# Performance work log

Hardware: AMD Instinct MI355X
Metric: run time of the kernel (lower is better)

The kernel has to match this reference:

```python
import jax, jax.numpy as jnp
import numpy as np

E = 7       # number of experts (len(expert_details))
K = 2       # top-k routing
CAP = 3072  # per-expert capacity ~ ceil(T*K/E * 1.25)
D = 1024    # d_model
H = 4096    # d_ff = 4*d_model
T = 8192    # tokens (B=2, S=4096)


def setup_inputs() -> dict:
    key = jax.random.key(0)
    k1, k2, k3, k4 = jax.random.split(key, 4)
    x = jax.random.normal(k1, (T, D), jnp.float32)
    Wg = jax.random.normal(k2, (D, E), jnp.float32) * 0.02
    W1 = jax.random.normal(k3, (E, D, H), jnp.float32) * 0.02
    W2 = jax.random.normal(k4, (E, H, D), jnp.float32) * 0.02
    return {"x": x, "Wg": Wg, "W1": W1, "W2": W2}


def reference(x, Wg, W1, W2):
    Tn, Dn = x.shape
    # --- router ---
    gates = jax.nn.softmax(x @ Wg, axis=-1)          # [T, E]
    topw, topi = jax.lax.top_k(gates, K)             # [T, K]
    topw = topw / jnp.sum(topw, axis=-1, keepdims=True)
    flat_e = topi.reshape(-1)                        # [T*K] expert ids (int)
    flat_w = topw.reshape(-1)                        # [T*K] combine weights
    # --- position within each expert (priority = token order) ---
    onehot = jax.nn.one_hot(flat_e, E, dtype=jnp.int32)           # [T*K, E]
    pos = jnp.sum(jnp.cumsum(onehot, axis=0) * onehot, axis=-1) - 1  # [T*K]
    keep = pos < CAP
    slot = jnp.where(keep, pos, CAP)  # overflow tokens go to pad slot CAP
    # --- dispatch: scatter tokens into [E, CAP, D] buffer ---
    x_rep = jnp.repeat(x, K, axis=0)                               # [T*K, D]
    buf = jnp.zeros((E, CAP + 1, Dn), x.dtype).at[flat_e, slot].set(x_rep)[:, :CAP]
    # --- grouped expert FFN (grouped GEMMs) ---
    h = jax.nn.gelu(jnp.einsum('ecd,edh->ech', buf, W1))
    y = jnp.einsum('ech,ehd->ecd', h, W2)                          # [E, CAP, D]
    # --- combine: gather back and weight ---
    y_pad = jnp.concatenate([y, jnp.zeros((E, 1, Dn), y.dtype)], axis=1)
    out_slots = y_pad[flat_e, slot] * (flat_w * keep.astype(flat_w.dtype))[:, None]
    return out_slots.reshape(Tn, K, Dn).sum(axis=1)                # [T, D]
```

## Files before the change

### kernel.cpp

```cpp
#include <hip/hip_runtime.h>
#include <stdint.h>


#define NEXP 7
#define KTOP 2
#define CAP 3072
#define DM 1024
#define HF 4096
#define TT 8192
#define RBLK 32

typedef __bf16 bf16x8 __attribute__((ext_vector_type(8)));
typedef float f32x4 __attribute__((ext_vector_type(4)));

__device__ __forceinline__ unsigned short f2bf(float v) {
  union { float f; unsigned u; } a; a.f = v;
  unsigned r = a.u + 0x7FFFu + ((a.u >> 16) & 1u);
  return (unsigned short)(r >> 16);
}
__device__ __forceinline__ float bf2f(unsigned short h) {
  union { unsigned u; float f; } a; a.u = ((unsigned)h) << 16; return a.f;
}
__device__ __forceinline__ float gelu_t(float v) {
  float u = 0.7978845608028654f * (v + 0.044715f * v * v * v);
  float ex = __expf(2.0f * u);
  float th = 1.0f - 2.0f / (ex + 1.0f);
  return 0.5f * v * (1.0f + th);
}
__device__ __forceinline__ void gl2lds16(const void* g, void* l) {
  __builtin_amdgcn_global_load_lds(
      (const __attribute__((address_space(1))) unsigned int*)g,
      (__attribute__((address_space(3))) unsigned int*)l, 16, 0, 0);
}

__global__ void init_counts(int* counts) {
  if (threadIdx.x < NEXP) counts[threadIdx.x] = 0;
}

__global__ __launch_bounds__(256) void router_fused(
    const float* __restrict__ x, const float* __restrict__ Wg,
    int* __restrict__ counts, int* __restrict__ flatSlot,
    int* __restrict__ tokOfSlot, float* __restrict__ wOfSlot,
    unsigned short* __restrict__ xb) {
  __shared__ float sWgT[NEXP][DM];
  __shared__ int hist[NEXP], base[NEXP];
  __shared__ int pickE[RBLK * 2];
  __shared__ int pickR[RBLK * 2];
  __shared__ float pickW[RBLK * 2];
  int tid = threadIdx.x, lane = tid & 63, wave = tid >> 6;

  for (int i = tid; i < NEXP * DM; i += 256) {
    int e = i / DM, d = i - e * DM;
    sWgT[e][d] = Wg[d * NEXP + e];
  }
  if (tid < NEXP) hist[tid] = 0;
  __syncthreads();

  for (int tt = wave; tt < RBLK; tt += 4) {
    int t = blockIdx.x * RBLK + tt;
    const float4* xr = (const float4*)(x + (long)t * DM);
    double acc[NEXP];
#pragma unroll
    for (int e = 0; e < NEXP; ++e) acc[e] = 0.0;
#pragma unroll
    for (int j = 0; j < 4; ++j) {
      float4 xv = xr[j * 64 + lane];
      int d4 = (j * 64 + lane) * 4;
#pragma unroll
      for (int e = 0; e < NEXP; ++e) {
        float4 wv = *(const float4*)&sWgT[e][d4];
        acc[e] += (double)xv.x * (double)wv.x + (double)xv.y * (double)wv.y
                + (double)xv.z * (double)wv.z + (double)xv.w * (double)wv.w;
      }
    }
#pragma unroll
    for (int e = 0; e < NEXP; ++e) {
#pragma unroll
      for (int off = 32; off > 0; off >>= 1) acc[e] += __shfl_down(acc[e], off);
    }
    if (lane == 0) {
      int i1 = 0; double l1 = acc[0];
      for (int e2 = 1; e2 < NEXP; ++e2) if (acc[e2] > l1) { l1 = acc[e2]; i1 = e2; }
      int i2 = -1; double l2 = -1e300;
      for (int e2 = 0; e2 < NEXP; ++e2) if (e2 != i1 && acc[e2] > l2) { l2 = acc[e2]; i2 = e2; }
      float w1 = (float)(1.0 / (1.0 + exp(l2 - l1)));
      int r0 = atomicAdd(&hist[i1], 1);
      int r1 = atomicAdd(&hist[i2], 1);
      pickE[2 * tt] = i1;     pickR[2 * tt] = r0;     pickW[2 * tt] = w1;
      pickE[2 * tt + 1] = i2; pickR[2 * tt + 1] = r1; pickW[2 * tt + 1] = 1.0f - w1;
    }
  }
  __syncthreads();
  if (tid < NEXP) base[tid] = atomicAdd(&counts[tid], hist[tid]);
  __syncthreads();

  for (int tt = wave; tt < RBLK; tt += 4) {
    int t = blockIdx.x * RBLK + tt;
    const float4* xr = (const float4*)(x + (long)t * DM);
    float4 v0 = xr[0 * 64 + lane], v1 = xr[1 * 64 + lane];
    float4 v2 = xr[2 * 64 + lane], v3 = xr[3 * 64 + lane];
    ushort4 o0, o1, o2, o3;
    o0.x = f2bf(v0.x); o0.y = f2bf(v0.y); o0.z = f2bf(v0.z); o0.w = f2bf(v0.w);
    o1.x = f2bf(v1.x); o1.y = f2bf(v1.y); o1.z = f2bf(v1.z); o1.w = f2bf(v1.w);
    o2.x = f2bf(v2.x); o2.y = f2bf(v2.y); o2.z = f2bf(v2.z); o2.w = f2bf(v2.w);
    o3.x = f2bf(v3.x); o3.y = f2bf(v3.y); o3.z = f2bf(v3.z); o3.w = f2bf(v3.w);
#pragma unroll
    for (int p = 0; p < 2; ++p) {
      int e = pickE[2 * tt + p];
      int s = base[e] + pickR[2 * tt + p];
      int fi = t * 2 + p;
      if (lane == 0) {
        flatSlot[fi] = (s < CAP) ? s : CAP;
        if (s < CAP) { tokOfSlot[e * CAP + s] = fi; wOfSlot[e * CAP + s] = pickW[2 * tt + p]; }
      }
      if (s < CAP) {
        ushort4* dst = (ushort4*)(xb + ((long)e * CAP + s) * DM);
        dst[0 * 64 + lane] = o0; dst[1 * 64 + lane] = o1;
        dst[2 * 64 + lane] = o2; dst[3 * 64 + lane] = o3;
      }
    }
  }
}

__global__ void transcvt(const float* __restrict__ in, unsigned short* __restrict__ out,
                         int R, int C) {
  __shared__ float tile[64][65];
  long base = (long)blockIdx.z * (long)R * (long)C;
  const float* inp = in + base;
  unsigned short* outp = out + base;
  int c0 = blockIdx.x * 64, r0 = blockIdx.y * 64;
  int lx = threadIdx.x & 63, ly = threadIdx.x >> 6;
#pragma unroll
  for (int i = 0; i < 16; ++i) {
    int r = ly + i * 4;
    tile[r][lx] = inp[(long)(r0 + r) * C + c0 + lx];
  }
  __syncthreads();
#pragma unroll
  for (int i = 0; i < 16; ++i) {
    int c = ly + i * 4;
    outp[(long)(c0 + c) * R + r0 + lx] = f2bf(tile[lx][c]);
  }
}

template <int EPI>
__global__ __launch_bounds__(512, 2) void gemm256(
    const unsigned short* __restrict__ A, const unsigned short* __restrict__ Bt,
    void* __restrict__ Cout, const int* __restrict__ counts,
    const int* __restrict__ tokOfSlot, const float* __restrict__ wOfSlot,
    int LD, int klen, int N, int kspl, long aexps, long cexps) {
  __shared__ __align__(16) unsigned short sAb[2][16384];
  __shared__ __align__(16) unsigned short sBb[2][16384];
  int e = blockIdx.z / kspl, ks = blockIdx.z % kspl;
  int mcnt = counts[e]; mcnt = mcnt < CAP ? mcnt : CAP;
  int m0 = blockIdx.y * 256;
  if (m0 >= mcnt) return;
  int n0 = blockIdx.x * 256;
  long kstart = (long)ks * klen;

  const unsigned short* Ae = A + (long)e * aexps;
  const unsigned short* Be = Bt + (long)e * (long)N * LD;

  int tid = threadIdx.x;
  int lane = tid & 63, wave = tid >> 6;
  int wr = wave >> 2, wc = wave & 3;
  int lm = lane & 15, quad = lane >> 4;

  int srow = tid >> 3;
  int scol = ((lane & 7) ^ (lane >> 3)) << 3;
  const unsigned short* As = Ae + (long)(m0 + srow) * LD + kstart + scol;
  const unsigned short* Bs = Be + (long)(n0 + srow) * LD + kstart + scol;

  int abase = (wr * 128 + lm) * 64;
  int bbase = (wc * 64 + lm) * 64;
  int cx0 = (quad ^ (lm & 7)) << 3;
  int cx1 = ((quad + 4) ^ (lm & 7)) << 3;

  f32x4 acc[8][4];
#pragma unroll
  for (int i = 0; i < 8; ++i)
#pragma unroll
    for (int j = 0; j < 4; ++j) acc[i][j] = f32x4{0.f, 0.f, 0.f, 0.f};

  int NT = klen >> 6, NI = NT >> 1;

#define STA(buf, kt, half) do { \
    int _kt = (kt) < NT ? (kt) : (NT - 1); \
    gl2lds16(As + (long)_kt * 64 + (long)((half) * 2) * 64 * LD, \
             &sAb[buf][(half) * 8192 + tid * 8]); \
    gl2lds16(As + (long)_kt * 64 + (long)((half) * 2 + 1) * 64 * LD, \
             &sAb[buf][(half) * 8192 + 4096 + tid * 8]); \
  } while (0)
#define STB(buf, kt, half) do { \
    int _kt = (kt) < NT ? (kt) : (NT - 1); \
    gl2lds16(Bs + (long)_kt * 64 + (long)((half) * 2) * 64 * LD, \
             &sBb[buf][(half) * 8192 + tid * 8]); \
    gl2lds16(Bs + (long)_kt * 64 + (long)((half) * 2 + 1) * 64 * LD, \
             &sBb[buf][(half) * 8192 + 4096 + tid * 8]); \
  } while (0)

  bf16x8 bF[4][2];

#define PHASE(buf, mi0, RB, STAGE, VM) do { \
    bf16x8 a00 = *(const bf16x8*)&sAb[buf][abase + (mi0) * 1024 + cx0]; \
    bf16x8 a01 = *(const bf16x8*)&sAb[buf][abase + (mi0) * 1024 + cx1]; \
    bf16x8 a10 = *(const bf16x8*)&sAb[buf][abase + (mi0) * 1024 + 1024 + cx0]; \
    bf16x8 a11 = *(const bf16x8*)&sAb[buf][abase + (mi0) * 1024 + 1024 + cx1]; \
    if (RB) { \
      _Pragma("unroll") \
      for (int ni = 0; ni < 4; ++ni) { \
        bF[ni][0] = *(const bf16x8*)&sBb[buf][bbase + ni * 1024 + cx0]; \
        bF[ni][1] = *(const bf16x8*)&sBb[buf][bbase + ni * 1024 + cx1]; \
      } \
    } \
    STAGE; \
    __builtin_amdgcn_s_barrier(); \
    asm volatile("s_waitcnt lgkmcnt(0)" ::: "memory"); \
    __builtin_amdgcn_sched_barrier(0); \
    __builtin_amdgcn_s_setprio(1); \
    _Pragma("unroll") \
    for (int ni = 0; ni < 4; ++ni) { \
      acc[mi0][ni]     = __builtin_amdgcn_mfma_f32_16x16x32_bf16(a00, bF[ni][0], acc[mi0][ni], 0, 0, 0); \
      acc[mi0][ni]     = __builtin_amdgcn_mfma_f32_16x16x32_bf16(a01, bF[ni][1], acc[mi0][ni], 0, 0, 0); \
      acc[mi0 + 1][ni] = __builtin_amdgcn_mfma_f32_16x16x32_bf16(a10, bF[ni][0], acc[mi0 + 1][ni], 0, 0, 0); \
      acc[mi0 + 1][ni] = __builtin_amdgcn_mfma_f32_16x16x32_bf16(a11, bF[ni][1], acc[mi0 + 1][ni], 0, 0, 0); \
    } \
    __builtin_amdgcn_s_setprio(0); \
    VM; \
    __builtin_amdgcn_s_barrier(); \
  } while (0)

  STA(0, 0, 0); STA(0, 0, 1); STB(0, 0, 0); STB(0, 0, 1);
  STB(1, 1, 0); STB(1, 1, 1);
  asm volatile("s_waitcnt vmcnt(4)" ::: "memory");
  __builtin_amdgcn_s_barrier();

  for (int t = 0; t < NI; ++t) {
    int k0 = 2 * t, k1 = 2 * t + 1;
    PHASE(0, 0, 1, STA(1, k1, 0), (void)0);
    PHASE(0, 2, 0, STA(1, k1, 1), (void)0);
    PHASE(0, 4, 0, STB(0, k0 + 2, 0), (void)0);
    PHASE(0, 6, 0, STB(0, k0 + 2, 1),
          asm volatile("s_waitcnt vmcnt(4)" ::: "memory"));
    PHASE(1, 0, 1, STA(0, k0 + 2, 0), (void)0);
    PHASE(1, 2, 0, STA(0, k0 + 2, 1), (void)0);
    PHASE(1, 4, 0, STB(1, k1 + 2, 0), (void)0);
    PHASE(1, 6, 0, STB(1, k1 + 2, 1),
          asm volatile("s_waitcnt vmcnt(4)" ::: "memory"));
  }
  asm volatile("s_waitcnt vmcnt(0)" ::: "memory");
#undef PHASE
#undef STA
#undef STB

  if (EPI == 0) {
    unsigned short* Ce = (unsigned short*)Cout + (long)e * cexps;
#pragma unroll
    for (int mi = 0; mi < 8; ++mi) {
      int mb = m0 + wr * 128 + mi * 16 + quad * 4;
#pragma unroll
      for (int r = 0; r < 4; ++r) {
        int m = mb + r;
        if (m < mcnt) {
#pragma unroll
          for (int ni = 0; ni < 4; ++ni) {
            int n = n0 + wc * 64 + ni * 16 + lm;
            Ce[(long)m * N + n] = f2bf(gelu_t(acc[mi][ni][r]));
          }
        }
      }
    }
  } else {
    unsigned short* Y = (unsigned short*)Cout + (long)ks * ((long)TT * KTOP * DM);
#pragma unroll
    for (int mi = 0; mi < 8; ++mi) {
      int mb = m0 + wr * 128 + mi * 16 + quad * 4;
#pragma unroll
      for (int r = 0; r < 4; ++r) {
        int m = mb + r;
        if (m < mcnt) {
          int fi = tokOfSlot[e * CAP + m];
          float w = wOfSlot[e * CAP + m];
#pragma unroll
          for (int ni = 0; ni < 4; ++ni) {
            int n = n0 + wc * 64 + ni * 16 + lm;
            Y[(long)fi * N + n] = f2bf(w * acc[mi][ni][r]);
          }
        }
      }
    }
  }
}

template <int EPI>
__global__ __launch_bounds__(256, 2) void gemm_bt(
    const unsigned short* __restrict__ A, const unsigned short* __restrict__ Bt,
    void* __restrict__ Cout, const int* __restrict__ counts,
    const int* __restrict__ tokOfSlot, const float* __restrict__ wOfSlot,
    int K, int N, int eoff, long aexps, long cexps) {
  __shared__ unsigned short sA[128 * 32];
  __shared__ unsigned short sB[128 * 32];
  int e = eoff + blockIdx.z;
  int mcnt = counts[e]; mcnt = mcnt < CAP ? mcnt : CAP;
  int m0 = blockIdx.y * 128;
  if (m0 >= mcnt) return;
  int n0 = blockIdx.x * 128;
  const unsigned short* Ae = A + (long)blockIdx.z * aexps;
  const unsigned short* Be = Bt + (long)e * (long)N * (long)K;

  int tid = threadIdx.x;
  int lane = tid & 63, wave = tid >> 6;
  int lm = lane & 15, quad = lane >> 4;
  int wm = (wave & 1) * 64, wn = (wave >> 1) * 64;

  int ra = tid >> 2;
  int ca = (tid & 3) * 8;
  const unsigned short* Ab0 = Ae + (long)(m0 + ra) * K + ca;
  const unsigned short* Ab1 = Ae + (long)(m0 + 64 + ra) * K + ca;
  const unsigned short* Bb0 = Be + (long)(n0 + ra) * K + ca;
  const unsigned short* Bb1 = Be + (long)(n0 + 64 + ra) * K + ca;
  unsigned short* sAp0 = &sA[tid * 8];
  unsigned short* sAp1 = &sA[(tid + 256) * 8];
  unsigned short* sBp0 = &sB[tid * 8];
  unsigned short* sBp1 = &sB[(tid + 256) * 8];

  f32x4 acc[4][4];
#pragma unroll
  for (int i = 0; i < 4; ++i)
#pragma unroll
    for (int j = 0; j < 4; ++j) acc[i][j] = f32x4{0.f, 0.f, 0.f, 0.f};

  for (int k0 = 0; k0 < K; k0 += 32) {
    gl2lds16(Ab0 + k0, sAp0);
    gl2lds16(Ab1 + k0, sAp1);
    gl2lds16(Bb0 + k0, sBp0);
    gl2lds16(Bb1 + k0, sBp1);
    __syncthreads();
    bf16x8 aF[4], bFf[4];
#pragma unroll
    for (int mi = 0; mi < 4; ++mi)
      aF[mi] = *(const bf16x8*)&sA[(wm + mi * 16 + lm) * 32 + quad * 8];
#pragma unroll
    for (int ni = 0; ni < 4; ++ni)
      bFf[ni] = *(const bf16x8*)&sB[(wn + ni * 16 + lm) * 32 + quad * 8];
#pragma unroll
    for (int mi = 0; mi < 4; ++mi)
#pragma unroll
      for (int ni = 0; ni < 4; ++ni)
        acc[mi][ni] = __builtin_amdgcn_mfma_f32_16x16x32_bf16(aF[mi], bFf[ni], acc[mi][ni], 0, 0, 0);
    __syncthreads();
  }

  if (EPI == 0) {
    unsigned short* Ce = (unsigned short*)Cout + (long)blockIdx.z * cexps;
#pragma unroll
    for (int mi = 0; mi < 4; ++mi) {
      int mb = m0 + wm + mi * 16 + quad * 4;
#pragma unroll
      for (int r = 0; r < 4; ++r) {
        int m = mb + r;
        if (m < mcnt) {
#pragma unroll
          for (int ni = 0; ni < 4; ++ni) {
            int n = n0 + wn + ni * 16 + lm;
            Ce[(long)m * N + n] = f2bf(gelu_t(acc[mi][ni][r]));
          }
        }
      }
    }
  } else {
    unsigned short* Y = (unsigned short*)Cout;
#pragma unroll
    for (int mi = 0; mi < 4; ++mi) {
      int mb = m0 + wm + mi * 16 + quad * 4;
#pragma unroll
      for (int r = 0; r < 4; ++r) {
        int m = mb + r;
        if (m < mcnt) {
          int fi = tokOfSlot[e * CAP + m];
          float w = wOfSlot[e * CAP + m];
#pragma unroll
          for (int ni = 0; ni < 4; ++ni) {
            int n = n0 + wn + ni * 16 + lm;
            Y[(long)fi * N + n] = f2bf(w * acc[mi][ni][r]);
          }
        }
      }
    }
  }
}

__global__ void combine_k2(const unsigned short* __restrict__ yflat,
                           const int* __restrict__ flatSlot, float* __restrict__ out) {
  int t = blockIdx.x;
  bool k0 = flatSlot[2 * t] < CAP, k1 = flatSlot[2 * t + 1] < CAP;
  const long S = (long)TT * KTOP * DM;
  const ushort4* y00 = (const ushort4*)(yflat + (long)(2 * t) * DM);
  const ushort4* y01 = (const ushort4*)(yflat + S + (long)(2 * t) * DM);
  const ushort4* y10 = (const ushort4*)(yflat + (long)(2 * t + 1) * DM);
  const ushort4* y11 = (const ushort4*)(yflat + S + (long)(2 * t + 1) * DM);
  ushort4 a = y00[threadIdx.x], a2 = y01[threadIdx.x];
  ushort4 b = y10[threadIdx.x], b2 = y11[threadIdx.x];
  float4 r;
  r.x = (k0 ? bf2f(a.x) + bf2f(a2.x) : 0.f) + (k1 ? bf2f(b.x) + bf2f(b2.x) : 0.f);
  r.y = (k0 ? bf2f(a.y) + bf2f(a2.y) : 0.f) + (k1 ? bf2f(b.y) + bf2f(b2.y) : 0.f);
  r.z = (k0 ? bf2f(a.z) + bf2f(a2.z) : 0.f) + (k1 ? bf2f(b.z) + bf2f(b2.z) : 0.f);
  r.w = (k0 ? bf2f(a.w) + bf2f(a2.w) : 0.f) + (k1 ? bf2f(b.w) + bf2f(b2.w) : 0.f);
  ((float4*)(out + (long)t * DM))[threadIdx.x] = r;
}

__global__ void combine_k(const unsigned short* __restrict__ yflat,
                          const int* __restrict__ flatSlot, float* __restrict__ out) {
  int t = blockIdx.x;
  bool k0 = flatSlot[2 * t] < CAP, k1 = flatSlot[2 * t + 1] < CAP;
  const ushort4* y0 = (const ushort4*)(yflat + (long)(2 * t) * DM);
  const ushort4* y1 = (const ushort4*)(yflat + (long)(2 * t + 1) * DM);
  ushort4 a = y0[threadIdx.x], b = y1[threadIdx.x];
  float4 r;
  r.x = (k0 ? bf2f(a.x) : 0.f) + (k1 ? bf2f(b.x) : 0.f);
  r.y = (k0 ? bf2f(a.y) : 0.f) + (k1 ? bf2f(b.y) : 0.f);
  r.z = (k0 ? bf2f(a.z) : 0.f) + (k1 ? bf2f(b.z) : 0.f);
  r.w = (k0 ? bf2f(a.w) : 0.f) + (k1 ? bf2f(b.w) : 0.f);
  ((float4*)(out + (long)t * DM))[threadIdx.x] = r;
}

extern "C" void kernel_launch(void* const* d_in, const int* in_sizes, int n_in,
                              void* d_out, int out_size, void* d_ws, size_t ws_size,
                              hipStream_t stream) {
  const float* x  = (const float*)d_in[0];
  const float* Wg = (const float*)d_in[1];
  const float* W1 = (const float*)d_in[2];
  const float* W2 = (const float*)d_in[3];
  float* out = (float*)d_out;

  char* ws = (char*)d_ws;
  size_t off = 0;
  auto alloc = [&](size_t b) { void* p = ws + off; off = (off + b + 255) & ~(size_t)255; return p; };
  int* counts            = (int*)alloc(NEXP * 4);
  int* flatSlot          = (int*)alloc((size_t)TT * KTOP * 4);
  int* tokOfSlot         = (int*)alloc((size_t)NEXP * CAP * 4);
  float* wOfSlot         = (float*)alloc((size_t)NEXP * CAP * 4);
  unsigned short* Wb1    = (unsigned short*)alloc((size_t)NEXP * DM * HF * 2);
  unsigned short* Wb2    = (unsigned short*)alloc((size_t)NEXP * DM * HF * 2);
  unsigned short* xb     = (unsigned short*)alloc((size_t)NEXP * CAP * DM * 2);
  unsigned short* yflat  = (unsigned short*)alloc((size_t)2 * TT * KTOP * DM * 2);
  size_t hbA = (size_t)NEXP * CAP * HF * 2;
  size_t hbB = (size_t)CAP * HF * 2;
  int planA = (off + hbA) <= ws_size;
  unsigned short* hb = (unsigned short*)alloc(planA ? hbA : hbB);

  init_counts<<<1, 64, 0, stream>>>(counts);
  router_fused<<<TT / RBLK, 256, 0, stream>>>(x, Wg, counts, flatSlot, tokOfSlot, wOfSlot, xb);
  transcvt<<<dim3(HF / 64, DM / 64, NEXP), 256, 0, stream>>>(W1, Wb1, DM, HF);
  transcvt<<<dim3(DM / 64, HF / 64, NEXP), 256, 0, stream>>>(W2, Wb2, HF, DM);

  if (planA) {
    gemm256<0><<<dim3(HF / 256, CAP / 256, NEXP), 512, 0, stream>>>(
        xb, Wb1, hb, counts, tokOfSlot, wOfSlot, DM, DM, HF, 1,
        (long)CAP * DM, (long)CAP * HF);
    gemm256<1><<<dim3(DM / 256, CAP / 256, NEXP * 2), 512, 0, stream>>>(
        hb, Wb2, yflat, counts, tokOfSlot, wOfSlot, HF, HF / 2, DM, 2,
        (long)CAP * HF, 0);
    combine_k2<<<TT, 256, 0, stream>>>(yflat, flatSlot, out);
  } else {
    for (int e = 0; e < NEXP; ++e) {
      gemm_bt<0><<<dim3(HF / 128, CAP / 128, 1), 256, 0, stream>>>(
          xb + (size_t)e * CAP * DM, Wb1, hb, counts, tokOfSlot, wOfSlot, DM, HF, e, 0, 0);
      gemm_bt<1><<<dim3(DM / 128, CAP / 128, 1), 256, 0, stream>>>(
          hb, Wb2, yflat, counts, tokOfSlot, wOfSlot, HF, DM, e, 0, 0);
    }
    combine_k<<<TT, 256, 0, stream>>>(yflat, flatSlot, out);
  }
}
```

Before: 782.6 us.

## Fuse combine into second expert GEMM via fp32 atomic adds to output

The second grouped GEMM's epilogue now atomically adds the weighted fp32 results straight into a pre-zeroed output row for each token, so the bf16 split-K staging buffer and the separate combine kernel are no longer needed. The weight transpose-convert kernel now writes four bf16 values per store instead of one, and a scheduling barrier is removed from the MFMA phase macro. The aim is to cut intermediate memory traffic and a kernel launch. In exchange it adds contended atomics, order-dependent summation, and a zeroing pass.

```diff
diff --git a/kernel.cpp b/kernel.cpp
--- a/kernel.cpp
+++ b/kernel.cpp
@@ -35,6 +35,10 @@
 
 __global__ void init_counts(int* counts) {
   if (threadIdx.x < NEXP) counts[threadIdx.x] = 0;
+}
+
+__global__ void zero_out(float* __restrict__ out) {
+  ((float4*)(out + (long)blockIdx.x * DM))[threadIdx.x] = float4{0.f, 0.f, 0.f, 0.f};
 }
 
 __global__ __launch_bounds__(256) void router_fused(
@@ -136,10 +140,17 @@
     tile[r][lx] = inp[(long)(r0 + r) * C + c0 + lx];
   }
   __syncthreads();
-#pragma unroll
-  for (int i = 0; i < 16; ++i) {
-    int c = ly + i * 4;
-    outp[(long)(c0 + c) * R + r0 + lx] = f2bf(tile[lx][c]);
+  int sx = threadIdx.x & 15;
+  int sy = threadIdx.x >> 4;
+#pragma unroll
+  for (int cc = 0; cc < 4; ++cc) {
+    int c = cc * 16 + sy;
+    ushort4 o;
+    o.x = f2bf(tile[4 * sx + 0][c]);
+    o.y = f2bf(tile[4 * sx + 1][c]);
+    o.z = f2bf(tile[4 * sx + 2][c]);
+    o.w = f2bf(tile[4 * sx + 3][c]);
+    *(ushort4*)&outp[(long)(c0 + c) * R + r0 + 4 * sx] = o;
   }
 }
 
@@ -216,7 +227,6 @@
     STAGE; \
     __builtin_amdgcn_s_barrier(); \
     asm volatile("s_waitcnt lgkmcnt(0)" ::: "memory"); \
-    __builtin_amdgcn_sched_barrier(0); \
     __builtin_amdgcn_s_setprio(1); \
     _Pragma("unroll") \
     for (int ni = 0; ni < 4; ++ni) { \
@@ -271,7 +281,7 @@
       }
     }
   } else {
-    unsigned short* Y = (unsigned short*)Cout + (long)ks * ((long)TT * KTOP * DM);
+    float* O = (float*)Cout;
 #pragma unroll
     for (int mi = 0; mi < 8; ++mi) {
       int mb = m0 + wr * 128 + mi * 16 + quad * 4;
@@ -281,10 +291,11 @@
         if (m < mcnt) {
           int fi = tokOfSlot[e * CAP + m];
           float w = wOfSlot[e * CAP + m];
+          long trow = (long)(fi >> 1) * N;
 #pragma unroll
           for (int ni = 0; ni < 4; ++ni) {
             int n = n0 + wc * 64 + ni * 16 + lm;
-            Y[(long)fi * N + n] = f2bf(w * acc[mi][ni][r]);
+            atomicAdd(&O[trow + n], w * acc[mi][ni][r]);
           }
         }
       }
@@ -390,25 +401,6 @@
   }
 }
 
-__global__ void combine_k2(const unsigned short* __restrict__ yflat,
-                           const int* __restrict__ flatSlot, float* __restrict__ out) {
-  int t = blockIdx.x;
-  bool k0 = flatSlot[2 * t] < CAP, k1 = flatSlot[2 * t + 1] < CAP;
-  const long S = (long)TT * KTOP * DM;
-  const ushort4* y00 = (const ushort4*)(yflat + (long)(2 * t) * DM);
-  const ushort4* y01 = (const ushort4*)(yflat + S + (long)(2 * t) * DM);
-  const ushort4* y10 = (const ushort4*)(yflat + (long)(2 * t + 1) * DM);
-  const ushort4* y11 = (const ushort4*)(yflat + S + (long)(2 * t + 1) * DM);
-  ushort4 a = y00[threadIdx.x], a2 = y01[threadIdx.x];
-  ushort4 b = y10[threadIdx.x], b2 = y11[threadIdx.x];
-  float4 r;
-  r.x = (k0 ? bf2f(a.x) + bf2f(a2.x) : 0.f) + (k1 ? bf2f(b.x) + bf2f(b2.x) : 0.f);
-  r.y = (k0 ? bf2f(a.y) + bf2f(a2.y) : 0.f) + (k1 ? bf2f(b.y) + bf2f(b2.y) : 0.f);
-  r.z = (k0 ? bf2f(a.z) + bf2f(a2.z) : 0.f) + (k1 ? bf2f(b.z) + bf2f(b2.z) : 0.f);
-  r.w = (k0 ? bf2f(a.w) + bf2f(a2.w) : 0.f) + (k1 ? bf2f(b.w) + bf2f(b2.w) : 0.f);
-  ((float4*)(out + (long)t * DM))[threadIdx.x] = r;
-}
-
 __global__ void combine_k(const unsigned short* __restrict__ yflat,
                           const int* __restrict__ flatSlot, float* __restrict__ out) {
   int t = blockIdx.x;
@@ -443,7 +435,7 @@
   unsigned short* Wb1    = (unsigned short*)alloc((size_t)NEXP * DM * HF * 2);
   unsigned short* Wb2    = (unsigned short*)alloc((size_t)NEXP * DM * HF * 2);
   unsigned short* xb     = (unsigned short*)alloc((size_t)NEXP * CAP * DM * 2);
-  unsigned short* yflat  = (unsigned short*)alloc((size_t)2 * TT * KTOP * DM * 2);
+  unsigned short* yflat  = (unsigned short*)alloc((size_t)TT * KTOP * DM * 2);
   size_t hbA = (size_t)NEXP * CAP * HF * 2;
   size_t hbB = (size_t)CAP * HF * 2;
   int planA = (off + hbA) <= ws_size;
@@ -455,13 +447,13 @@
   transcvt<<<dim3(DM / 64, HF / 64, NEXP), 256, 0, stream>>>(W2, Wb2, HF, DM);
 
   if (planA) {
+    zero_out<<<TT, 256, 0, stream>>>(out);
     gemm256<0><<<dim3(HF / 256, CAP / 256, NEXP), 512, 0, stream>>>(
         xb, Wb1, hb, counts, tokOfSlot, wOfSlot, DM, DM, HF, 1,
         (long)CAP * DM, (long)CAP * HF);
     gemm256<1><<<dim3(DM / 256, CAP / 256, NEXP * 2), 512, 0, stream>>>(
-        hb, Wb2, yflat, counts, tokOfSlot, wOfSlot, HF, HF / 2, DM, 2,
+        hb, Wb2, out, counts, tokOfSlot, wOfSlot, HF, HF / 2, DM, 2,
         (long)CAP * HF, 0);
-    combine_k2<<<TT, 256, 0, stream>>>(yflat, flatSlot, out);
   } else {
     for (int e = 0; e < NEXP; ++e) {
       gemm_bt<0><<<dim3(HF / 128, CAP / 128, 1), 256, 0, stream>>>(
```

Result: slower. 827.7 us (+5.8%).
